# Kernel tuning notes

Measured on AMD Instinct MI355X. Metric: run time of the kernel, lower is better.

## Reference

```python
import jax, jax.numpy as jnp
import numpy as np

DIM = 1024
H = 16
HKV = 4
HD = DIM // H  # 64
GROUP = H // HKV
ROPE_BASE = 10000.0
B, T = 2, 2048


def rms_norm(x, eps):
    return x * jax.lax.rsqrt(jnp.mean(x * x, axis=-1, keepdims=True) + eps)


def apply_rotary(x, cos, sin):
    # x: [B, h, T, HD]; cos/sin: [1, 1, T, HD//2]
    half = x.shape[-1] // 2
    x1, x2 = x[..., :half], x[..., half:]
    return jnp.concatenate([x1 * cos + x2 * sin, -x1 * sin + x2 * cos], axis=-1)


def setup_inputs() -> dict:
    key = jax.random.key(0)
    ks = jax.random.split(key, 5)
    s = 0.02
    return {
        "x": jax.random.normal(ks[0], (B, T, DIM), dtype=jnp.float32),
        "Wq": jax.random.normal(ks[1], (DIM, DIM), dtype=jnp.float32) * s,
        "Wk": jax.random.normal(ks[2], (HKV * HD, DIM), dtype=jnp.float32) * s,
        "Wv": jax.random.normal(ks[3], (HKV * HD, DIM), dtype=jnp.float32) * s,
        "Wproj": jax.random.normal(ks[4], (DIM, DIM), dtype=jnp.float32) * s,
        "q_gain": jnp.full((H,), 12.0, dtype=jnp.float32),
    }


def reference(x, Wq, Wk, Wv, Wproj, q_gain):
    bsz, seqlen, dim = x.shape
    eps = jnp.asarray(jnp.finfo(x.dtype).eps, x.dtype)

    # double RMSNorm path: normalized input for q/k, raw input for v
    x_qk = rms_norm(x, eps)
    q = (x_qk @ Wq.T).reshape(bsz, seqlen, H, HD).transpose(0, 2, 1, 3)    # [B,H,T,D]
    k = (x_qk @ Wk.T).reshape(bsz, seqlen, HKV, HD).transpose(0, 2, 1, 3)  # [B,Hkv,T,D]
    v = (x @ Wv.T).reshape(bsz, seqlen, HKV, HD).transpose(0, 2, 1, 3)     # [B,Hkv,T,D]

    q = rms_norm(q, eps)
    k = rms_norm(k, eps)

    # rotary embeddings
    t = jnp.arange(seqlen, dtype=jnp.float32)
    inv_freq = 1.0 / (ROPE_BASE ** (jnp.arange(0, HD, 2, dtype=jnp.float32) / HD))
    freqs = jnp.outer(t, inv_freq)                       # [T, HD//2]
    cos = jnp.cos(freqs)[None, None].astype(x.dtype)
    sin = jnp.sin(freqs)[None, None].astype(x.dtype)
    q = apply_rotary(q, cos, sin)
    k = apply_rotary(k, cos, sin)

    # per-head gain on q
    q = q * q_gain.astype(q.dtype)[None, :, None, None]

    # GQA: expand kv heads to query heads
    k_r = jnp.repeat(k, GROUP, axis=1)  # [B,H,T,D]
    v_r = jnp.repeat(v, GROUP, axis=1)

    scale = 1.0 / np.sqrt(HD)
    scores = jnp.einsum("bhqd,bhkd->bhqk", q, k_r) * scale
    causal = jnp.tril(jnp.ones((seqlen, seqlen), dtype=bool))
    scores = jnp.where(causal[None, None], scores, jnp.asarray(-jnp.inf, scores.dtype))
    attn = jax.nn.softmax(scores, axis=-1)
    y = jnp.einsum("bhqk,bhkd->bhqd", attn, v_r)          # [B,H,T,D]

    # XSA: remove value-direction component from output
    y_bt = y.transpose(0, 2, 1, 3)                        # [B,T,H,D]
    v_bt = v.transpose(0, 2, 1, 3)                        # [B,T,Hkv,D]
    y_g = y_bt.reshape(bsz, seqlen, HKV, GROUP, HD)
    vnorm = jnp.sqrt(jnp.sum(v_bt * v_bt, axis=-1, keepdims=True))
    vn = (v_bt / jnp.maximum(vnorm, 1e-12))[..., None, :]  # [B,T,Hkv,1,D]
    proj = jnp.sum(y_g * vn, axis=-1, keepdims=True) * vn
    y_bt = (y_g - proj).reshape(bsz, seqlen, H, HD)

    return y_bt.reshape(bsz, seqlen, dim) @ Wproj.T
```

## Files before the change

### kernel.cpp

```cpp
#include <hip/hip_runtime.h>
#include <hip/hip_bf16.h>

typedef __attribute__((ext_vector_type(8))) short bf8v;
typedef __attribute__((ext_vector_type(4))) float f4v;
typedef __attribute__((ext_vector_type(4))) unsigned u4v;

#define MFMA16(a,b,c) __builtin_amdgcn_mfma_f32_16x16x32_bf16((a),(b),(c),0,0,0)

#define GLD16(gp, lp) __builtin_amdgcn_global_load_lds( \
    (const __attribute__((address_space(1))) void*)(gp), \
    (__attribute__((address_space(3))) void*)(lp), 16, 0, 0)

#define DIMC   1024
#define TSEQ   2048
#define NH     16
#define NKV    4
#define HDIM   64
#define RMS_EPS 1.1920929e-07f
#define QSCALE 0.1803368801111601f

__device__ __forceinline__ ushort f2bf(float f) {
  unsigned u = __builtin_bit_cast(unsigned, f);
  u = (u + 0x7FFFu + ((u >> 16) & 1u)) >> 16;
  return (ushort)u;
}
__device__ __forceinline__ float bf2f(ushort u) {
  return __builtin_bit_cast(float, (unsigned)u << 16);
}
__device__ __forceinline__ unsigned cvtpk(float lo, float hi) {
  unsigned r;
  asm("v_cvt_pk_bf16_f32 %0, %1, %2" : "=v"(r) : "v"(lo), "v"(hi));
  return r;
}

__global__ __launch_bounds__(256) void prep_all(
    const float* __restrict__ x,
    const float* __restrict__ Wq, const float* __restrict__ Wk,
    const float* __restrict__ Wv, const float* __restrict__ Wp,
    ushort* __restrict__ xhi, ushort* __restrict__ xlo,
    ushort* __restrict__ xb,
    ushort* __restrict__ wqkh, ushort* __restrict__ wqkl,
    ushort* __restrict__ wvb, ushort* __restrict__ wpb,
    float* __restrict__ cosT, float* __restrict__ sinT) {
  __shared__ float red[4];
  int bid = blockIdx.x, tid = threadIdx.x;
  if (bid < 4096) {
    int row = bid;
    int lane = tid & 63, w = tid >> 6;
    float4 v = ((const float4*)(x + (size_t)row * DIMC))[tid];
    float ss = v.x * v.x + v.y * v.y + v.z * v.z + v.w * v.w;
    for (int off = 32; off; off >>= 1) ss += __shfl_xor(ss, off);
    if (lane == 0) red[w] = ss;
    __syncthreads();
    float tot = red[0] + red[1] + red[2] + red[3];
    float rs = rsqrtf(tot * (1.0f / DIMC) + RMS_EPS);
    float n0 = v.x * rs, n1 = v.y * rs, n2 = v.z * rs, n3 = v.w * rs;
    ushort4 h, l, ob;
    h.x = f2bf(n0); l.x = f2bf(n0 - bf2f(h.x));
    h.y = f2bf(n1); l.y = f2bf(n1 - bf2f(h.y));
    h.z = f2bf(n2); l.z = f2bf(n2 - bf2f(h.z));
    h.w = f2bf(n3); l.w = f2bf(n3 - bf2f(h.w));
    ob.x = f2bf(v.x); ob.y = f2bf(v.y); ob.z = f2bf(v.z); ob.w = f2bf(v.w);
    ((ushort4*)(xhi + (size_t)row * DIMC))[tid] = h;
    ((ushort4*)(xlo + (size_t)row * DIMC))[tid] = l;
    ((ushort4*)(xb  + (size_t)row * DIMC))[tid] = ob;
    return;
  }
  int wb = bid - 4096;
  if (wb < 1280) {
    const float* src;
    size_t si, di;
    if (wb < 1024) { src = Wq; si = (size_t)wb * 256 + tid; di = si; }
    else { src = Wk; si = (size_t)(wb - 1024) * 256 + tid; di = 262144 + si; }
    float4 v = ((const float4*)src)[si];
    ushort4 h, l;
    h.x = f2bf(v.x); l.x = f2bf(v.x - bf2f(h.x));
    h.y = f2bf(v.y); l.y = f2bf(v.y - bf2f(h.y));
    h.z = f2bf(v.z); l.z = f2bf(v.z - bf2f(h.z));
    h.w = f2bf(v.w); l.w = f2bf(v.w - bf2f(h.w));
    ((ushort4*)wqkh)[di] = h;
    ((ushort4*)wqkl)[di] = l;
  } else if (wb < 2560) {
    const float* src;
    ushort* dst;
    int i;
    if (wb < 1536) { src = Wv; dst = wvb; i = (wb - 1280) * 256 + tid; }
    else           { src = Wp; dst = wpb; i = (wb - 1536) * 256 + tid; }
    float4 v = ((const float4*)src)[i];
    ushort4 o;
    o.x = f2bf(v.x); o.y = f2bf(v.y); o.z = f2bf(v.z); o.w = f2bf(v.w);
    ((ushort4*)dst)[i] = o;
  } else {
    int i = (wb - 2560) * 256 + tid;
    int t = i >> 5, j = i & 31;
    float inv = 1.0f / powf(10000.0f, (float)j * (1.0f / 32.0f));
    float f = (float)t * inv;
    cosT[i] = cosf(f);
    sinT[i] = sinf(f);
  }
}

__global__ __launch_bounds__(256, 3)
void gemm_qkv(const ushort* __restrict__ xhi, const ushort* __restrict__ xlo,
              const ushort* __restrict__ wqkh, const ushort* __restrict__ wqkl,
              float* __restrict__ QKf, ushort* __restrict__ QKc,
              const ushort* __restrict__ xb, const ushort* __restrict__ wvb,
              float* __restrict__ Vf) {
  __shared__ __align__(16) ushort lA[128 * 64];
  __shared__ __align__(16) ushort lB[128 * 64];
  const int bid = blockIdx.x;
  int u;
  bool big;
  if (bid < 256)      { big = true;  u = bid; }
  else if (bid < 448) { big = false; u = bid - 256; }
  else if (bid < 512) { big = true;  u = 256 + (bid - 448); }
  else                { big = false; u = 192 + (bid - 512); }

  const ushort *Ap0, *Bp0, *Ap1, *Bp1;
  float* Cf = QKf;
  int N = 1280, nsteps, mt, n0;
  if (big) {
    mt = u / 10; n0 = (u % 10) * 128;
    Ap0 = xlo; Bp0 = wqkh; Ap1 = xhi; Bp1 = wqkl; nsteps = 32;
  } else if (u < 320) {
    mt = u / 10; n0 = (u % 10) * 128;
    Ap0 = xhi; Bp0 = wqkh; Ap1 = Ap0; Bp1 = Bp0; nsteps = 16;
  } else {
    int v = u - 320; mt = v >> 1; n0 = (v & 1) * 128;
    Ap0 = xb; Bp0 = wvb; Ap1 = Ap0; Bp1 = Bp0; nsteps = 16;
    Cf = Vf; N = 256;
  }
  const int m0 = mt * 128;

  const int t = threadIdx.x;
  const int lane = t & 63, w = t >> 6;
  const int wr = w >> 1, wc = w & 1;
  const int l15 = lane & 15, lg = lane >> 4;
  const int srow = t >> 3, scp = t & 7;

  f4v acc[4][4] = {};

  for (int s = 0; s < nsteps; ++s) {
    const ushort* Ab = (s < 16) ? Ap0 : Ap1;
    const ushort* Bb = (s < 16) ? Bp0 : Bp1;
    const int kk = (s & 15) * 64;
    for (int i = 0; i < 4; ++i) {
      int row = srow + i * 32;
      int sc = scp ^ (row & 7);
      const ushort* ga = Ab + (size_t)(m0 + row) * DIMC + kk + sc * 8;
      const ushort* gb = Bb + (size_t)(n0 + row) * DIMC + kk + sc * 8;
      GLD16(ga, &lA[w * 512 + i * 2048]);
      GLD16(gb, &lB[w * 512 + i * 2048]);
    }
    __syncthreads();
    for (int kx = 0; kx < 2; ++kx) {
      bf8v af[4], bfr[4];
      for (int m = 0; m < 4; ++m) {
        int row = wr * 64 + m * 16 + l15;
        int ch = (kx * 4 + lg) ^ (row & 7);
        af[m] = *(const bf8v*)&lA[row * 64 + ch * 8];
      }
      for (int n = 0; n < 4; ++n) {
        int row = wc * 64 + n * 16 + l15;
        int ch = (kx * 4 + lg) ^ (row & 7);
        bfr[n] = *(const bf8v*)&lB[row * 64 + ch * 8];
      }
      for (int m = 0; m < 4; ++m)
        for (int n = 0; n < 4; ++n)
          acc[m][n] = MFMA16(af[m], bfr[n], acc[m][n]);
    }
    __syncthreads();
  }

  if (big) {
    for (int m = 0; m < 4; ++m)
      for (int n = 0; n < 4; ++n)
        for (int j = 0; j < 4; ++j) {
          int r = m0 + wr * 64 + m * 16 + lg * 4 + j;
          int c = n0 + wc * 64 + n * 16 + l15;
          QKc[(size_t)r * 1280 + c] = f2bf(acc[m][n][j]);
        }
  } else {
    for (int m = 0; m < 4; ++m)
      for (int n = 0; n < 4; ++n)
        for (int j = 0; j < 4; ++j) {
          int r = m0 + wr * 64 + m * 16 + lg * 4 + j;
          int c = n0 + wc * 64 + n * 16 + l15;
          Cf[(size_t)r * N + c] = acc[m][n][j];
        }
  }
}

__global__ __launch_bounds__(256, 4)
void gemm_bt(const ushort* __restrict__ A0, const ushort* __restrict__ B0,
             float* __restrict__ C, int N) {
  __shared__ __align__(16) ushort lA[64 * 64];
  __shared__ __align__(16) ushort lB[64 * 64];
  const int t = threadIdx.x;
  const int lane = t & 63, w = t >> 6;
  const int l15 = lane & 15, lg = lane >> 4;
  const int m0 = blockIdx.y * 64, n0 = blockIdx.x * 64;
  const int srow = t >> 3, scp = t & 7;

  f4v acc[4] = {};

  for (int k0 = 0; k0 < 1024; k0 += 64) {
    for (int i = 0; i < 2; ++i) {
      int row = srow + i * 32;
      int sc = scp ^ (row & 7);
      GLD16(A0 + (size_t)(m0 + row) * DIMC + k0 + sc * 8,
            &lA[w * 512 + i * 2048]);
      GLD16(B0 + (size_t)(n0 + row) * DIMC + k0 + sc * 8,
            &lB[w * 512 + i * 2048]);
    }
    __syncthreads();
    for (int kx = 0; kx < 2; ++kx) {
      int arow = w * 16 + l15;
      int ach = (kx * 4 + lg) ^ (arow & 7);
      bf8v af = *(const bf8v*)&lA[arow * 64 + ach * 8];
      for (int n = 0; n < 4; ++n) {
        int row = n * 16 + l15;
        int ch = (kx * 4 + lg) ^ (row & 7);
        bf8v bfr = *(const bf8v*)&lB[row * 64 + ch * 8];
        acc[n] = MFMA16(af, bfr, acc[n]);
      }
    }
    __syncthreads();
  }

  for (int n = 0; n < 4; ++n)
    for (int j = 0; j < 4; ++j) {
      int r = m0 + w * 16 + lg * 4 + j;
      int c = n0 + n * 16 + l15;
      C[(size_t)r * N + c] = acc[n][j];
    }
}

__global__ __launch_bounds__(256) void post_all(
    const float* __restrict__ QKf, const ushort* __restrict__ QKc,
    const float* __restrict__ cosT,
    const float* __restrict__ sinT, const float* __restrict__ qgain,
    ushort* __restrict__ qhi, ushort* __restrict__ qlo,
    ushort* __restrict__ kb16,
    const float* __restrict__ Vf, ushort* __restrict__ vt2,
    ushort* __restrict__ vhat_q) {
  __shared__ float lds[64][69];
  __shared__ float rnv[64];
  int bid = blockIdx.x;
  if (bid < 4096) {
    int m = bid;
    int b = m >> 11, tpos = m & 2047;
    int lane = threadIdx.x & 63, w = threadIdx.x >> 6;
    int d = lane, j = d & 31;
    float sgn = (d < 32) ? 1.0f : -1.0f;
    float c = cosT[tpos * 32 + j], s = sinT[tpos * 32 + j];

    for (int i = 0; i < 4; ++i) {
      int h = w * 4 + i;
      size_t base = (size_t)m * 1280 + h * HDIM + d;
      float q = QKf[base] + bf2f(QKc[base]);
      float ss = q * q;
      for (int off = 32; off; off >>= 1) ss += __shfl_xor(ss, off);
      float rs = rsqrtf(ss * (1.0f / HDIM) + RMS_EPS);
      float qn = q * rs;
      float partner = __shfl_xor(qn, 32);
      float ro = (qn * c + sgn * partner * s) * (qgain[h] * QSCALE);
      ushort hi = f2bf(ro);
      ushort lo = f2bf(ro - bf2f(hi));
      size_t idx = (((size_t)b * NH + h) * TSEQ + tpos) * HDIM + d;
      qhi[idx] = hi;
      qlo[idx] = lo;
    }
    {
      int kv = w;
      size_t base = (size_t)m * 1280 + 1024 + kv * HDIM + d;
      float k = QKf[base] + bf2f(QKc[base]);
      float ss = k * k;
      for (int off = 32; off; off >>= 1) ss += __shfl_xor(ss, off);
      float rs = rsqrtf(ss * (1.0f / HDIM) + RMS_EPS);
      float kn = k * rs;
      float partner = __shfl_xor(kn, 32);
      float ro = kn * c + sgn * partner * s;
      kb16[((size_t)(b * NKV + kv) * TSEQ + tpos) * HDIM + d] = f2bf(ro);
    }
    return;
  }
  {
    int vb = bid - 4096;
    int bkv = vb >> 5, tt = vb & 31;
    int b = bkv >> 2, kv = bkv & 3;
    int tid = threadIdx.x;
    for (int i = 0; i < 16; ++i) {
      int idx = i * 256 + tid;
      int tloc = idx >> 6, d = idx & 63;
      lds[d][tloc] = Vf[((size_t)(b * TSEQ + tt * 64 + tloc)) * 256 + kv * 64 + d];
    }
    __syncthreads();
    {
      int t = tid >> 2, prt = tid & 3;
      float ssum = 0.f;
      for (int dd = 0; dd < 16; ++dd) {
        float v = lds[prt * 16 + dd][t];
        ssum += v * v;
      }
      ssum += __shfl_xor(ssum, 1);
      ssum += __shfl_xor(ssum, 2);
      if (prt == 0) rnv[t] = 1.0f / fmaxf(sqrtf(ssum), 1e-12f);
    }
    __syncthreads();
    for (int i = 0; i < 16; ++i) {
      int idx = i * 256 + tid;
      int d = idx >> 6, tloc = idx & 63;
      vt2[(size_t)bkv * (TSEQ * 64) + tt * 4096 + d * 64 + tloc] = f2bf(lds[d][tloc]);
    }
    for (int i = 0; i < 16; ++i) {
      int idx = i * 256 + tid;
      int tloc = idx >> 6, d = idx & 63;
      vhat_q[((size_t)bkv * TSEQ + tt * 64 + tloc) * 64 + d] =
          f2bf(lds[d][tloc] * rnv[tloc]);
    }
  }
}

#define E(s,t,k,l) ((unsigned)(s) | ((unsigned)(t) << 8) | \
                    ((unsigned)(k) << 16) | ((unsigned)(l) << 24))
__global__ __launch_bounds__(256, 5) void attn_chunk(
    const ushort* __restrict__ qhi, const ushort* __restrict__ qlo,
    const ushort* __restrict__ kb16, const ushort* __restrict__ vt2,
    ushort* __restrict__ pyb, float* __restrict__ pml) {
  static const unsigned LUT[80] = {
    E(76,31,0,8), E(77,31,8,8), E(78,31,16,8), E(79,31,24,8),
    E(72,30,0,8), E(73,30,8,8), E(74,30,16,8),
    E(68,29,0,8), E(69,29,8,8), E(64,28,0,8),
    E(45,23,0,8), E(46,23,8,8), E(47,23,16,8),
    E(42,22,0,8), E(43,22,8,8), E(39,21,0,8),
    E(22,15,0,8), E(23,15,8,8), E(20,14,0,8), E(7,7,0,8),
    E(75,30,24,7), E(70,29,16,7), E(71,29,23,7),
    E(65,28,8,7), E(66,28,15,7), E(67,28,22,7),
    E(60,27,0,7), E(61,27,7,7), E(62,27,14,7), E(63,27,21,7),
    E(56,26,0,7), E(57,26,7,7), E(58,26,14,7),
    E(52,25,0,7), E(53,25,7,7), E(48,24,0,7),
    E(44,22,16,7), E(40,21,8,7), E(41,21,15,7),
    E(36,20,0,7), E(37,20,7,7), E(38,20,14,7),
    E(33,19,0,7), E(34,19,7,7), E(30,18,0,7),
    E(21,14,8,7), E(18,13,0,7), E(19,13,7,7), E(16,12,0,7), E(6,6,0,7),
    E(59,26,21,6), E(54,25,14,6), E(55,25,20,6),
    E(49,24,7,6), E(50,24,13,6), E(51,24,19,6),
    E(35,19,14,6), E(31,18,7,6), E(32,18,13,6),
    E(27,17,0,6), E(28,17,6,6), E(29,17,12,6),
    E(24,16,0,6), E(25,16,6,6),
    E(17,12,7,6), E(14,11,0,6), E(15,11,6,6), E(12,10,0,6), E(5,5,0,6),
    E(26,16,12,5), E(13,10,6,5), E(10,9,0,5), E(11,9,5,5),
    E(8,8,0,5), E(4,4,0,5),
    E(9,8,5,4), E(3,3,0,4),
    E(2,2,0,3), E(1,1,0,2), E(0,0,0,1)
  };
  __shared__ __align__(16) ushort lk[2][64 * 64];
  __shared__ __align__(16) ushort lv[2][64 * 64];
  const int t = threadIdx.x;
  const int lane = t & 63, w = t >> 6;
  const int bid = blockIdx.x;
  const int combo = bid & 31;
  const unsigned e = LUT[bid >> 5];
  const int slot = e & 255;
  const int tile = (e >> 8) & 31;
  const int kb0 = (e >> 16) & 31;
  const int len = (int)(e >> 24);

  const int xcd = combo & 7, g = (combo >> 3) & 3;
  const int b = xcd >> 2, kv = xcd & 3, h = kv * 4 + g;
  const int l15 = lane & 15, lg = lane >> 4;
  const int q0 = tile * 64 + w * 16;
  const int t3 = t >> 3, tc8 = t & 7;
  const int rx = l15 & 7;
  const bool odd = (lg & 1);

  const size_t qoff = (((size_t)(b * NH + h)) * TSEQ + q0 + l15) * HDIM;
  bf8v bq0h = *(const bf8v*)(qhi + qoff + lg * 8);
  bf8v bq1h = *(const bf8v*)(qhi + qoff + 32 + lg * 8);
  bf8v bq0l = *(const bf8v*)(qlo + qoff + lg * 8);
  bf8v bq1l = *(const bf8v*)(qlo + qoff + 32 + lg * 8);

  const ushort* kb = kb16 + (size_t)(b * NKV + kv) * TSEQ * 64;
  const ushort* vb = vt2 + (size_t)(b * NKV + kv) * TSEQ * 64;

#define STAGE(BUF, KT) do { \
    _Pragma("unroll") \
    for (int i = 0; i < 2; ++i) { \
      int row = i * 32 + t3; \
      int sc = tc8 ^ (row & 7); \
      GLD16(kb + (size_t)((KT) * 64 + row) * 64 + sc * 8, \
            &lk[BUF][(i * 32 + (w << 3)) * 64]); \
      GLD16(vb + (size_t)(KT) * 4096 + row * 64 + sc * 8, \
            &lv[BUF][(i * 32 + (w << 3)) * 64]); \
    } } while (0)

  STAGE(0, kb0);

  f4v y[4] = {};
  f4v lsum = {};
  float mrow = 0.f;
  const short ob16 = (short)0x3F80;
  const bf8v onesv = { ob16, ob16, ob16, ob16, ob16, ob16, ob16, ob16 };

#pragma unroll 1
  for (int itc = 0; itc < len; ++itc) {
    const int cur = itc & 1;
    const int kt = kb0 + itc;
    __syncthreads();
    if (itc + 1 < len) STAGE(cur ^ 1, kt + 1);

    const ushort* lkc = &lk[cur][0];
    const ushort* lvc = &lv[cur][0];
    const int kv0 = kt * 64;

    f4v s4[4];
    const f4v zi = { -mrow, -mrow, -mrow, -mrow };
    __builtin_amdgcn_s_setprio(1);
#pragma unroll
    for (int n = 0; n < 4; ++n) {
      const ushort* krow = lkc + (n * 16 + l15) * 64;
      bf8v kh0 = *(const bf8v*)&krow[((0 + lg) ^ rx) * 8];
      bf8v kh1 = *(const bf8v*)&krow[((4 + lg) ^ rx) * 8];
      f4v acc = MFMA16(kh0, bq0h, zi);
      acc = MFMA16(kh1, bq1h, acc);
      acc = MFMA16(kh0, bq0l, acc);
      acc = MFMA16(kh1, bq1l, acc);
      s4[n] = acc;
    }
    __builtin_amdgcn_s_setprio(0);

    const bool need_mask = (kt == tile);
    float mloc = -1e30f;
#pragma unroll
    for (int n = 0; n < 4; ++n)
#pragma unroll
      for (int j = 0; j < 4; ++j) {
        float v = s4[n][j];
        if (need_mask && (kv0 + n * 16 + lg * 4 + j > q0 + l15)) v = -1e30f;
        s4[n][j] = v;
        mloc = fmaxf(mloc, v);
      }
    if (__any(mloc > 11.5f)) {
      float mf = fmaxf(mloc, __shfl_xor(mloc, 16));
      mf = fmaxf(mf, __shfl_xor(mf, 32));
      float delta = fmaxf(mf, 0.f);
      float scf = exp2f(-delta);
      lsum *= scf;
#pragma unroll
      for (int n = 0; n < 4; ++n) y[n] *= scf;
#pragma unroll
      for (int n = 0; n < 4; ++n)
#pragma unroll
        for (int j = 0; j < 4; ++j) s4[n][j] -= delta;
      mrow += delta;
    }
#pragma unroll
    for (int n = 0; n < 4; ++n)
#pragma unroll
      for (int j = 0; j < 4; ++j)
        s4[n][j] = exp2f(s4[n][j]);

    unsigned d0a = cvtpk(s4[0][0], s4[0][1]), d0b = cvtpk(s4[0][2], s4[0][3]);
    unsigned d1a = cvtpk(s4[1][0], s4[1][1]), d1b = cvtpk(s4[1][2], s4[1][3]);
    unsigned d2a = cvtpk(s4[2][0], s4[2][1]), d2b = cvtpk(s4[2][2], s4[2][3]);
    unsigned d3a = cvtpk(s4[3][0], s4[3][1]), d3b = cvtpk(s4[3][2], s4[3][3]);
    asm("v_permlane32_swap_b32 %0, %1" : "+v"(d0a), "+v"(d1a));
    asm("v_permlane32_swap_b32 %0, %1" : "+v"(d0b), "+v"(d1b));
    asm("v_permlane32_swap_b32 %0, %1" : "+v"(d2a), "+v"(d3a));
    asm("v_permlane32_swap_b32 %0, %1" : "+v"(d2b), "+v"(d3b));
    unsigned sa0 = (unsigned)__shfl_xor((int)d0a, 16);
    unsigned sb0 = (unsigned)__shfl_xor((int)d1a, 16);
    unsigned sa1 = (unsigned)__shfl_xor((int)d0b, 16);
    unsigned sb1 = (unsigned)__shfl_xor((int)d1b, 16);
    unsigned sa2 = (unsigned)__shfl_xor((int)d2a, 16);
    unsigned sb2 = (unsigned)__shfl_xor((int)d3a, 16);
    unsigned sa3 = (unsigned)__shfl_xor((int)d2b, 16);
    unsigned sb3 = (unsigned)__shfl_xor((int)d3b, 16);
    u4v u0 = { odd ? sb0 : d0a, odd ? sb1 : d0b,
               odd ? d1a : sa0, odd ? d1b : sa1 };
    u4v u1 = { odd ? sb2 : d2a, odd ? sb3 : d2b,
               odd ? d3a : sa2, odd ? d3b : sa3 };
    bf8v pb0 = __builtin_bit_cast(bf8v, u0);
    bf8v pb1 = __builtin_bit_cast(bf8v, u1);

    __builtin_amdgcn_s_setprio(1);
#pragma unroll
    for (int n = 0; n < 4; ++n) {
      const ushort* vrow = lvc + (n * 16 + l15) * 64;
      bf8v va0 = *(const bf8v*)&vrow[((0 + lg) ^ rx) * 8];
      bf8v va1 = *(const bf8v*)&vrow[((4 + lg) ^ rx) * 8];
      y[n] = MFMA16(va0, pb0, y[n]);
      y[n] = MFMA16(va1, pb1, y[n]);
    }
    lsum = MFMA16(onesv, pb0, lsum);
    lsum = MFMA16(onesv, pb1, lsum);
    __builtin_amdgcn_s_setprio(0);
  }
#undef STAGE

  {
    const float lrow = lsum[0];
    const int pslot = combo * 80 + slot;
    ushort* pb = pyb + (size_t)pslot * 4096;
    const int q = w * 16 + l15;
#pragma unroll
    for (int n = 0; n < 4; ++n) {
      uint2 pk;
      pk.x = cvtpk(y[n][0], y[n][1]);
      pk.y = cvtpk(y[n][2], y[n][3]);
      *(uint2*)&pb[q * 64 + n * 16 + lg * 4] = pk;
    }
    if (lane < 16) {
      float* mlp = pml + (size_t)pslot * 128;
      mlp[q] = mrow;
      mlp[64 + q] = lrow;
    }
  }
}
#undef E

__global__ __launch_bounds__(256) void combine_kern(
    const ushort* __restrict__ pyb, const float* __restrict__ pml,
    const ushort* __restrict__ vhat_q, ushort* __restrict__ ytil) {
  const int bid = blockIdx.x;
  const int combo = bid & 31, tile = bid >> 5;
  const int xcd = combo & 7, g = (combo >> 3) & 3;
  const int b = xcd >> 2, kv = xcd & 3, h = kv * 4 + g;
  const int nch = (tile + 8) >> 3;
  const int sb = (tile < 8) ? tile
               : (tile < 16) ? 8 + ((tile - 8) << 1)
               : (tile < 24) ? 24 + 3 * (tile - 16)
                             : 48 + ((tile - 24) << 2);
  const int tid = threadIdx.x;
  const int q = tid >> 2, ds = (tid & 3) * 16;
  const int q0 = tile * 64;

  float m[4], l[4];
#pragma unroll
  for (int ci = 0; ci < 4; ++ci) {
    if (ci < nch) {
      const float* mlp = pml + (size_t)(combo * 80 + sb + ci) * 128;
      m[ci] = mlp[q];
      l[ci] = mlp[64 + q];
    } else { m[ci] = -1e30f; l[ci] = 0.f; }
  }
  float M = fmaxf(fmaxf(m[0], m[1]), fmaxf(m[2], m[3]));
  float y[16] = {};
  float ltot = 0.f;
#pragma unroll
  for (int ci = 0; ci < 4; ++ci) {
    if (ci < nch) {
      float sc = exp2f(m[ci] - M);
      ltot += l[ci] * sc;
      const ushort* pb = pyb + (size_t)(combo * 80 + sb + ci) * 4096 + q * 64 + ds;
      bf8v p0 = *(const bf8v*)pb;
      bf8v p1 = *(const bf8v*)(pb + 8);
#pragma unroll
      for (int dd = 0; dd < 8; ++dd) {
        y[dd] += sc * bf2f((ushort)p0[dd]);
        y[8 + dd] += sc * bf2f((ushort)p1[dd]);
      }
    }
  }
  float inv = 1.0f / fmaxf(ltot, 1e-37f);
  const ushort* vh = vhat_q + ((size_t)(b * NKV + kv) * TSEQ + q0 + q) * 64 + ds;
  bf8v v0 = *(const bf8v*)vh;
  bf8v v1 = *(const bf8v*)(vh + 8);
  float vv[16];
  float dp = 0.f;
#pragma unroll
  for (int dd = 0; dd < 8; ++dd) {
    vv[dd] = bf2f((ushort)v0[dd]);
    vv[8 + dd] = bf2f((ushort)v1[dd]);
  }
#pragma unroll
  for (int dd = 0; dd < 16; ++dd) {
    y[dd] *= inv;
    dp += y[dd] * vv[dd];
  }
  dp += __shfl_xor(dp, 1);
  dp += __shfl_xor(dp, 2);
  bf8v o0, o1;
#pragma unroll
  for (int dd = 0; dd < 8; ++dd) {
    o0[dd] = (short)f2bf(y[dd] - dp * vv[dd]);
    o1[dd] = (short)f2bf(y[8 + dd] - dp * vv[8 + dd]);
  }
  ushort* yo = ytil + ((size_t)(b * TSEQ + q0 + q)) * DIMC + h * HDIM + ds;
  *(bf8v*)yo = o0;
  *(bf8v*)(yo + 8) = o1;
}

extern "C" void kernel_launch(void* const* d_in, const int* in_sizes, int n_in,
                              void* d_out, int out_size, void* d_ws, size_t ws_size,
                              hipStream_t stream) {
  (void)in_sizes; (void)n_in; (void)out_size; (void)ws_size;
  const float* x  = (const float*)d_in[0];
  const float* Wq = (const float*)d_in[1];
  const float* Wk = (const float*)d_in[2];
  const float* Wv = (const float*)d_in[3];
  const float* Wp = (const float*)d_in[4];
  const float* qg = (const float*)d_in[5];
  float* out = (float*)d_out;
  char* ws = (char*)d_ws;
  const size_t KB = 1024, MB = 1ull << 20;

  ushort* xhi = (ushort*)(ws);
  ushort* xlo = (ushort*)(ws + 8 * MB);
  ushort* xb  = (ushort*)(ws + 16 * MB);
  ushort* wqkh = (ushort*)(ws + 24 * MB);
  ushort* wqkl = (ushort*)(ws + 26 * MB + 512 * KB);
  ushort* wvb = (ushort*)(ws + 29 * MB);
  ushort* wpb = (ushort*)(ws + 29 * MB + 512 * KB);
  float*  cosT = (float*)(ws + 31 * MB + 512 * KB);
  float*  sinT = (float*)(ws + 31 * MB + 768 * KB);
  float*  QKf  = (float*)(ws + 32 * MB);
  ushort* kb16 = (ushort*)(ws + 52 * MB);
  ushort* vt2  = (ushort*)(ws + 54 * MB);

  float*  Vf   = out;
  ushort* QKc  = (ushort*)((char*)out + 4 * MB);
  ushort* vhat_q = (ushort*)((char*)out + 14 * MB);
  ushort* qhb  = xhi;
  ushort* qlb  = xlo;
  ushort* ytil = xb;
  ushort* pyb = (ushort*)(ws + 32 * MB);
  float*  pml = (float*)(ws + 56 * MB);

  prep_all<<<6912, 256, 0, stream>>>(x, Wq, Wk, Wv, Wp, xhi, xlo, xb,
                                     wqkh, wqkl, wvb, wpb, cosT, sinT);

  gemm_qkv<<<704, 256, 0, stream>>>(xhi, xlo, wqkh, wqkl, QKf, QKc,
                                    xb, wvb, Vf);

  post_all<<<4352, 256, 0, stream>>>(QKf, QKc, cosT, sinT, qg, qhb, qlb, kb16,
                                     Vf, vt2, vhat_q);
  attn_chunk<<<2560, 256, 0, stream>>>(qhb, qlb, kb16, vt2, pyb, pml);
  combine_kern<<<1024, 256, 0, stream>>>(pyb, pml, vhat_q, ytil);
  gemm_bt<<<dim3(16, 64), 256, 0, stream>>>(ytil, wpb, out, 1024);
}
```

Before: 140.2 us.

## Enlarge attention query tile to 128 rows with 512-thread blocks

The chunked attention kernel now processes 128 query rows per block using 8 waves, so each staged K/V tile in LDS is reused by twice as many queries and the number of blocks and partial slots is halved. The chunk LUT and the combine kernel indexing are rewritten for 16 tiles of 128 rows with 40 slots per head combo. Waves whose queries lie entirely before the current key block skip compute, which adds per-wave imbalance on the diagonal tiles and a larger per-block register and occupancy footprint.

```diff
diff --git a/kernel.cpp b/kernel.cpp
--- a/kernel.cpp
+++ b/kernel.cpp
@@ -324,36 +324,31 @@
 
 #define E(s,t,k,l) ((unsigned)(s) | ((unsigned)(t) << 8) | \
                     ((unsigned)(k) << 16) | ((unsigned)(l) << 24))
-__global__ __launch_bounds__(256, 5) void attn_chunk(
+__global__ __launch_bounds__(512, 8) void attn_chunk(
     const ushort* __restrict__ qhi, const ushort* __restrict__ qlo,
     const ushort* __restrict__ kb16, const ushort* __restrict__ vt2,
     ushort* __restrict__ pyb, float* __restrict__ pml) {
-  static const unsigned LUT[80] = {
-    E(76,31,0,8), E(77,31,8,8), E(78,31,16,8), E(79,31,24,8),
-    E(72,30,0,8), E(73,30,8,8), E(74,30,16,8),
-    E(68,29,0,8), E(69,29,8,8), E(64,28,0,8),
-    E(45,23,0,8), E(46,23,8,8), E(47,23,16,8),
-    E(42,22,0,8), E(43,22,8,8), E(39,21,0,8),
-    E(22,15,0,8), E(23,15,8,8), E(20,14,0,8), E(7,7,0,8),
-    E(75,30,24,7), E(70,29,16,7), E(71,29,23,7),
-    E(65,28,8,7), E(66,28,15,7), E(67,28,22,7),
-    E(60,27,0,7), E(61,27,7,7), E(62,27,14,7), E(63,27,21,7),
-    E(56,26,0,7), E(57,26,7,7), E(58,26,14,7),
-    E(52,25,0,7), E(53,25,7,7), E(48,24,0,7),
-    E(44,22,16,7), E(40,21,8,7), E(41,21,15,7),
-    E(36,20,0,7), E(37,20,7,7), E(38,20,14,7),
-    E(33,19,0,7), E(34,19,7,7), E(30,18,0,7),
-    E(21,14,8,7), E(18,13,0,7), E(19,13,7,7), E(16,12,0,7), E(6,6,0,7),
-    E(59,26,21,6), E(54,25,14,6), E(55,25,20,6),
-    E(49,24,7,6), E(50,24,13,6), E(51,24,19,6),
-    E(35,19,14,6), E(31,18,7,6), E(32,18,13,6),
-    E(27,17,0,6), E(28,17,6,6), E(29,17,12,6),
-    E(24,16,0,6), E(25,16,6,6),
-    E(17,12,7,6), E(14,11,0,6), E(15,11,6,6), E(12,10,0,6), E(5,5,0,6),
-    E(26,16,12,5), E(13,10,6,5), E(10,9,0,5), E(11,9,5,5),
-    E(8,8,0,5), E(4,4,0,5),
-    E(9,8,5,4), E(3,3,0,4),
-    E(2,2,0,3), E(1,1,0,2), E(0,0,0,1)
+  static const unsigned LUT[40] = {
+    E(36,15,0,8), E(37,15,8,8), E(38,15,16,8), E(39,15,24,8),
+    E(32,14,0,8), E(33,14,8,8),
+    E(21,11,0,8), E(22,11,8,8), E(23,11,16,8),
+    E(18,10,0,8),
+    E(10,7,0,8), E(11,7,8,8),
+    E(3,3,0,8),
+    E(34,14,16,7), E(35,14,23,7),
+    E(28,13,0,7), E(29,13,7,7), E(30,13,14,7), E(31,13,21,7),
+    E(24,12,0,7), E(25,12,7,7),
+    E(19,10,8,7), E(20,10,15,7),
+    E(15,9,0,7), E(16,9,7,7),
+    E(8,6,0,7), E(9,6,7,7),
+    E(26,12,14,6), E(27,12,20,6),
+    E(17,9,14,6),
+    E(12,8,0,6), E(13,8,6,6), E(14,8,12,6),
+    E(6,5,0,6), E(7,5,6,6),
+    E(2,2,0,6),
+    E(4,4,0,5), E(5,4,5,5),
+    E(1,1,0,4),
+    E(0,0,0,2)
   };
   __shared__ __align__(16) ushort lk[2][64 * 64];
   __shared__ __align__(16) ushort lv[2][64 * 64];
@@ -370,8 +365,9 @@
   const int xcd = combo & 7, g = (combo >> 3) & 3;
   const int b = xcd >> 2, kv = xcd & 3, h = kv * 4 + g;
   const int l15 = lane & 15, lg = lane >> 4;
-  const int q0 = tile * 64 + w * 16;
-  const int t3 = t >> 3, tc8 = t & 7;
+  const int q0 = tile * 128 + w * 16;
+  const int ktLast = (q0 + 15) >> 6;
+  const int srow = t >> 3, sc8 = (t & 7);
   const int rx = l15 & 7;
   const bool odd = (lg & 1);
 
@@ -385,15 +381,12 @@
   const ushort* vb = vt2 + (size_t)(b * NKV + kv) * TSEQ * 64;
 
 #define STAGE(BUF, KT) do { \
-    _Pragma("unroll") \
-    for (int i = 0; i < 2; ++i) { \
-      int row = i * 32 + t3; \
-      int sc = tc8 ^ (row & 7); \
-      GLD16(kb + (size_t)((KT) * 64 + row) * 64 + sc * 8, \
-            &lk[BUF][(i * 32 + (w << 3)) * 64]); \
-      GLD16(vb + (size_t)(KT) * 4096 + row * 64 + sc * 8, \
-            &lv[BUF][(i * 32 + (w << 3)) * 64]); \
-    } } while (0)
+    int sc = sc8 ^ (srow & 7); \
+    GLD16(kb + (size_t)((KT) * 64 + srow) * 64 + sc * 8, \
+          &lk[BUF][w << 9]); \
+    GLD16(vb + (size_t)(KT) * 4096 + srow * 64 + sc * 8, \
+          &lv[BUF][w << 9]); \
+  } while (0)
 
   STAGE(0, kb0);
 
@@ -410,111 +403,113 @@
     __syncthreads();
     if (itc + 1 < len) STAGE(cur ^ 1, kt + 1);
 
-    const ushort* lkc = &lk[cur][0];
-    const ushort* lvc = &lv[cur][0];
-    const int kv0 = kt * 64;
-
-    f4v s4[4];
-    const f4v zi = { -mrow, -mrow, -mrow, -mrow };
-    __builtin_amdgcn_s_setprio(1);
-#pragma unroll
-    for (int n = 0; n < 4; ++n) {
-      const ushort* krow = lkc + (n * 16 + l15) * 64;
-      bf8v kh0 = *(const bf8v*)&krow[((0 + lg) ^ rx) * 8];
-      bf8v kh1 = *(const bf8v*)&krow[((4 + lg) ^ rx) * 8];
-      f4v acc = MFMA16(kh0, bq0h, zi);
-      acc = MFMA16(kh1, bq1h, acc);
-      acc = MFMA16(kh0, bq0l, acc);
-      acc = MFMA16(kh1, bq1l, acc);
-      s4[n] = acc;
-    }
-    __builtin_amdgcn_s_setprio(0);
-
-    const bool need_mask = (kt == tile);
-    float mloc = -1e30f;
-#pragma unroll
-    for (int n = 0; n < 4; ++n)
-#pragma unroll
-      for (int j = 0; j < 4; ++j) {
-        float v = s4[n][j];
-        if (need_mask && (kv0 + n * 16 + lg * 4 + j > q0 + l15)) v = -1e30f;
-        s4[n][j] = v;
-        mloc = fmaxf(mloc, v);
-      }
-    if (__any(mloc > 11.5f)) {
-      float mf = fmaxf(mloc, __shfl_xor(mloc, 16));
-      mf = fmaxf(mf, __shfl_xor(mf, 32));
-      float delta = fmaxf(mf, 0.f);
-      float scf = exp2f(-delta);
-      lsum *= scf;
-#pragma unroll
-      for (int n = 0; n < 4; ++n) y[n] *= scf;
+    if (kt <= ktLast) {
+      const ushort* lkc = &lk[cur][0];
+      const ushort* lvc = &lv[cur][0];
+      const int kv0 = kt * 64;
+
+      f4v s4[4];
+      const f4v zi = { -mrow, -mrow, -mrow, -mrow };
+      __builtin_amdgcn_s_setprio(1);
+#pragma unroll
+      for (int n = 0; n < 4; ++n) {
+        const ushort* krow = lkc + (n * 16 + l15) * 64;
+        bf8v kh0 = *(const bf8v*)&krow[((0 + lg) ^ rx) * 8];
+        bf8v kh1 = *(const bf8v*)&krow[((4 + lg) ^ rx) * 8];
+        f4v acc = MFMA16(kh0, bq0h, zi);
+        acc = MFMA16(kh1, bq1h, acc);
+        acc = MFMA16(kh0, bq0l, acc);
+        acc = MFMA16(kh1, bq1l, acc);
+        s4[n] = acc;
+      }
+      __builtin_amdgcn_s_setprio(0);
+
+      const bool need_mask = (kt == ktLast);
+      float mloc = -1e30f;
 #pragma unroll
       for (int n = 0; n < 4; ++n)
 #pragma unroll
-        for (int j = 0; j < 4; ++j) s4[n][j] -= delta;
-      mrow += delta;
-    }
-#pragma unroll
-    for (int n = 0; n < 4; ++n)
-#pragma unroll
-      for (int j = 0; j < 4; ++j)
-        s4[n][j] = exp2f(s4[n][j]);
-
-    unsigned d0a = cvtpk(s4[0][0], s4[0][1]), d0b = cvtpk(s4[0][2], s4[0][3]);
-    unsigned d1a = cvtpk(s4[1][0], s4[1][1]), d1b = cvtpk(s4[1][2], s4[1][3]);
-    unsigned d2a = cvtpk(s4[2][0], s4[2][1]), d2b = cvtpk(s4[2][2], s4[2][3]);
-    unsigned d3a = cvtpk(s4[3][0], s4[3][1]), d3b = cvtpk(s4[3][2], s4[3][3]);
-    asm("v_permlane32_swap_b32 %0, %1" : "+v"(d0a), "+v"(d1a));
-    asm("v_permlane32_swap_b32 %0, %1" : "+v"(d0b), "+v"(d1b));
-    asm("v_permlane32_swap_b32 %0, %1" : "+v"(d2a), "+v"(d3a));
-    asm("v_permlane32_swap_b32 %0, %1" : "+v"(d2b), "+v"(d3b));
-    unsigned sa0 = (unsigned)__shfl_xor((int)d0a, 16);
-    unsigned sb0 = (unsigned)__shfl_xor((int)d1a, 16);
-    unsigned sa1 = (unsigned)__shfl_xor((int)d0b, 16);
-    unsigned sb1 = (unsigned)__shfl_xor((int)d1b, 16);
-    unsigned sa2 = (unsigned)__shfl_xor((int)d2a, 16);
-    unsigned sb2 = (unsigned)__shfl_xor((int)d3a, 16);
-    unsigned sa3 = (unsigned)__shfl_xor((int)d2b, 16);
-    unsigned sb3 = (unsigned)__shfl_xor((int)d3b, 16);
-    u4v u0 = { odd ? sb0 : d0a, odd ? sb1 : d0b,
-               odd ? d1a : sa0, odd ? d1b : sa1 };
-    u4v u1 = { odd ? sb2 : d2a, odd ? sb3 : d2b,
-               odd ? d3a : sa2, odd ? d3b : sa3 };
-    bf8v pb0 = __builtin_bit_cast(bf8v, u0);
-    bf8v pb1 = __builtin_bit_cast(bf8v, u1);
-
-    __builtin_amdgcn_s_setprio(1);
-#pragma unroll
-    for (int n = 0; n < 4; ++n) {
-      const ushort* vrow = lvc + (n * 16 + l15) * 64;
-      bf8v va0 = *(const bf8v*)&vrow[((0 + lg) ^ rx) * 8];
-      bf8v va1 = *(const bf8v*)&vrow[((4 + lg) ^ rx) * 8];
-      y[n] = MFMA16(va0, pb0, y[n]);
-      y[n] = MFMA16(va1, pb1, y[n]);
-    }
-    lsum = MFMA16(onesv, pb0, lsum);
-    lsum = MFMA16(onesv, pb1, lsum);
-    __builtin_amdgcn_s_setprio(0);
+        for (int j = 0; j < 4; ++j) {
+          float v = s4[n][j];
+          if (need_mask && (kv0 + n * 16 + lg * 4 + j > q0 + l15)) v = -1e30f;
+          s4[n][j] = v;
+          mloc = fmaxf(mloc, v);
+        }
+      if (__any(mloc > 11.5f)) {
+        float mf = fmaxf(mloc, __shfl_xor(mloc, 16));
+        mf = fmaxf(mf, __shfl_xor(mf, 32));
+        float delta = fmaxf(mf, 0.f);
+        float scf = exp2f(-delta);
+        lsum *= scf;
+#pragma unroll
+        for (int n = 0; n < 4; ++n) y[n] *= scf;
+#pragma unroll
+        for (int n = 0; n < 4; ++n)
+#pragma unroll
+          for (int j = 0; j < 4; ++j) s4[n][j] -= delta;
+        mrow += delta;
+      }
+#pragma unroll
+      for (int n = 0; n < 4; ++n)
+#pragma unroll
+        for (int j = 0; j < 4; ++j)
+          s4[n][j] = exp2f(s4[n][j]);
+
+      unsigned d0a = cvtpk(s4[0][0], s4[0][1]), d0b = cvtpk(s4[0][2], s4[0][3]);
+      unsigned d1a = cvtpk(s4[1][0], s4[1][1]), d1b = cvtpk(s4[1][2], s4[1][3]);
+      unsigned d2a = cvtpk(s4[2][0], s4[2][1]), d2b = cvtpk(s4[2][2], s4[2][3]);
+      unsigned d3a = cvtpk(s4[3][0], s4[3][1]), d3b = cvtpk(s4[3][2], s4[3][3]);
+      asm("v_permlane32_swap_b32 %0, %1" : "+v"(d0a), "+v"(d1a));
+      asm("v_permlane32_swap_b32 %0, %1" : "+v"(d0b), "+v"(d1b));
+      asm("v_permlane32_swap_b32 %0, %1" : "+v"(d2a), "+v"(d3a));
+      asm("v_permlane32_swap_b32 %0, %1" : "+v"(d2b), "+v"(d3b));
+      unsigned sa0 = (unsigned)__shfl_xor((int)d0a, 16);
+      unsigned sb0 = (unsigned)__shfl_xor((int)d1a, 16);
+      unsigned sa1 = (unsigned)__shfl_xor((int)d0b, 16);
+      unsigned sb1 = (unsigned)__shfl_xor((int)d1b, 16);
+      unsigned sa2 = (unsigned)__shfl_xor((int)d2a, 16);
+      unsigned sb2 = (unsigned)__shfl_xor((int)d3a, 16);
+      unsigned sa3 = (unsigned)__shfl_xor((int)d2b, 16);
+      unsigned sb3 = (unsigned)__shfl_xor((int)d3b, 16);
+      u4v u0 = { odd ? sb0 : d0a, odd ? sb1 : d0b,
+                 odd ? d1a : sa0, odd ? d1b : sa1 };
+      u4v u1 = { odd ? sb2 : d2a, odd ? sb3 : d2b,
+                 odd ? d3a : sa2, odd ? d3b : sa3 };
+      bf8v pb0 = __builtin_bit_cast(bf8v, u0);
+      bf8v pb1 = __builtin_bit_cast(bf8v, u1);
+
+      __builtin_amdgcn_s_setprio(1);
+#pragma unroll
+      for (int n = 0; n < 4; ++n) {
+        const ushort* vrow = lvc + (n * 16 + l15) * 64;
+        bf8v va0 = *(const bf8v*)&vrow[((0 + lg) ^ rx) * 8];
+        bf8v va1 = *(const bf8v*)&vrow[((4 + lg) ^ rx) * 8];
+        y[n] = MFMA16(va0, pb0, y[n]);
+        y[n] = MFMA16(va1, pb1, y[n]);
+      }
+      lsum = MFMA16(onesv, pb0, lsum);
+      lsum = MFMA16(onesv, pb1, lsum);
+      __builtin_amdgcn_s_setprio(0);
+    }
   }
 #undef STAGE
 
   {
     const float lrow = lsum[0];
-    const int pslot = combo * 80 + slot;
-    ushort* pb = pyb + (size_t)pslot * 4096;
-    const int q = w * 16 + l15;
+    const int pslot = combo * 40 + slot;
+    ushort* pb = pyb + (size_t)pslot * 8192;
+    const int qp = w * 16 + l15;
 #pragma unroll
     for (int n = 0; n < 4; ++n) {
       uint2 pk;
       pk.x = cvtpk(y[n][0], y[n][1]);
       pk.y = cvtpk(y[n][2], y[n][3]);
-      *(uint2*)&pb[q * 64 + n * 16 + lg * 4] = pk;
+      *(uint2*)&pb[qp * 64 + n * 16 + lg * 4] = pk;
     }
     if (lane < 16) {
-      float* mlp = pml + (size_t)pslot * 128;
-      mlp[q] = mrow;
-      mlp[64 + q] = lrow;
+      float* mlp = pml + (size_t)pslot * 256;
+      mlp[qp] = mrow;
+      mlp[128 + qp] = lrow;
     }
   }
 }
@@ -524,25 +519,27 @@
     const ushort* __restrict__ pyb, const float* __restrict__ pml,
     const ushort* __restrict__ vhat_q, ushort* __restrict__ ytil) {
   const int bid = blockIdx.x;
-  const int combo = bid & 31, tile = bid >> 5;
+  const int combo = bid & 31, ht = bid >> 5;
+  const int tile = ht >> 1;
   const int xcd = combo & 7, g = (combo >> 3) & 3;
   const int b = xcd >> 2, kv = xcd & 3, h = kv * 4 + g;
-  const int nch = (tile + 8) >> 3;
-  const int sb = (tile < 8) ? tile
-               : (tile < 16) ? 8 + ((tile - 8) << 1)
-               : (tile < 24) ? 24 + 3 * (tile - 16)
-                             : 48 + ((tile - 24) << 2);
+  const int nch = (tile >> 2) + 1;
+  const int sb = (tile < 4) ? tile
+               : (tile < 8) ? 4 + 2 * (tile - 4)
+               : (tile < 12) ? 12 + 3 * (tile - 8)
+                             : 24 + 4 * (tile - 12);
   const int tid = threadIdx.x;
   const int q = tid >> 2, ds = (tid & 3) * 16;
-  const int q0 = tile * 64;
+  const int qp = (ht & 1) * 64 + q;
+  const int q0 = ht * 64;
 
   float m[4], l[4];
 #pragma unroll
   for (int ci = 0; ci < 4; ++ci) {
     if (ci < nch) {
-      const float* mlp = pml + (size_t)(combo * 80 + sb + ci) * 128;
-      m[ci] = mlp[q];
-      l[ci] = mlp[64 + q];
+      const float* mlp = pml + (size_t)(combo * 40 + sb + ci) * 256;
+      m[ci] = mlp[qp];
+      l[ci] = mlp[128 + qp];
     } else { m[ci] = -1e30f; l[ci] = 0.f; }
   }
   float M = fmaxf(fmaxf(m[0], m[1]), fmaxf(m[2], m[3]));
@@ -553,7 +550,7 @@
     if (ci < nch) {
       float sc = exp2f(m[ci] - M);
       ltot += l[ci] * sc;
-      const ushort* pb = pyb + (size_t)(combo * 80 + sb + ci) * 4096 + q * 64 + ds;
+      const ushort* pb = pyb + (size_t)(combo * 40 + sb + ci) * 8192 + qp * 64 + ds;
       bf8v p0 = *(const bf8v*)pb;
       bf8v p1 = *(const bf8v*)(pb + 8);
 #pragma unroll
@@ -636,7 +633,7 @@
 
   post_all<<<4352, 256, 0, stream>>>(QKf, QKc, cosT, sinT, qg, qhb, qlb, kb16,
                                      Vf, vt2, vhat_q);
-  attn_chunk<<<2560, 256, 0, stream>>>(qhb, qlb, kb16, vt2, pyb, pml);
+  attn_chunk<<<1280, 512, 0, stream>>>(qhb, qlb, kb16, vt2, pyb, pml);
   combine_kern<<<1024, 256, 0, stream>>>(pyb, pml, vhat_q, ytil);
   gemm_bt<<<dim3(16, 64), 256, 0, stream>>>(ytil, wpb, out, 1024);
 }
```

After: 213.7 us. 1.52x slower.
